# Optimization experiments

Measured on AMD Instinct MI355X. Metric: run time of the kernel, lower is better.

## Reference

```python
import jax, jax.numpy as jnp
import numpy as np

B, C, K, D = 16, 128, 128, 256
EPS = 1e-5  # torch BatchNorm1d default eps


def _bn(x, gamma, beta):
    # torch BatchNorm1d training-mode on (N, ch, L): normalize each channel over (N, L)
    mean = x.mean(axis=(0, 2), keepdims=True)
    var = x.var(axis=(0, 2), keepdims=True)  # biased, matches torch normalization
    return (x - mean) / jnp.sqrt(var + EPS) * gamma[None, :, None] + beta[None, :, None]


def setup_inputs() -> dict:
    key = jax.random.key(0)
    ks = jax.random.split(key, 6)
    q = jax.random.normal(ks[0], (B, C, D), jnp.float32)
    kc = jax.random.normal(ks[1], (B, K, D), jnp.float32)
    W0 = jax.random.normal(ks[2], (D, D), jnp.float32) / np.sqrt(D)
    W1 = jax.random.normal(ks[3], (D, D), jnp.float32) / np.sqrt(D)
    cmask = jax.random.randint(ks[4], (B, C), 0, 2, jnp.int32)
    kmask = jax.random.randint(ks[5], (B, K), 0, 2, jnp.int32)
    klen = jnp.maximum(kmask.sum(axis=1), 1).astype(jnp.int32)
    return {
        "query_candidates_repr": q,
        "key_candidates": kc,
        "W0": W0,
        "W1": W1,
        "bn0_gamma": jnp.ones((C,), jnp.float32),
        "bn0_beta": jnp.zeros((C,), jnp.float32),
        "bn1_gamma": jnp.ones((K,), jnp.float32),
        "bn1_beta": jnp.zeros((K,), jnp.float32),
        "query_candidate_mask": cmask,
        "key_candidate_mask": kmask,
        "key_candidate_len": klen,
    }


def reference(query_candidates_repr, key_candidates, W0, W1,
              bn0_gamma, bn0_beta, bn1_gamma, bn1_beta,
              query_candidate_mask, key_candidate_mask, key_candidate_len):
    # gated_attention branch (att_type != 'softmax'), activate = tanh
    g0 = _bn(query_candidates_repr @ W0.T, bn0_gamma, bn0_beta)  # (B,C,D)
    g1 = _bn(key_candidates @ W1.T, bn1_gamma, bn1_beta)          # (B,K,D)
    # (B,C,K,D) gate product
    attention_weight = jax.nn.sigmoid(g1)[:, None, :, :] * jax.nn.sigmoid(g0)[:, :, None, :]
    attention_res = key_candidates[:, None, :, :] * attention_weight  # (B,C,K,D)
    mask = (query_candidate_mask[:, :, None] * key_candidate_mask[:, None, :]).astype(jnp.float32)
    attention_res_masked = attention_res * mask[..., None]
    attention_vector = attention_res_masked.sum(axis=2) / key_candidate_len[:, None, None].astype(jnp.float32)
    output_res = jnp.tanh(attention_vector)  # (B,C,D)
    return output_res, attention_res_masked, attention_weight.mean(axis=-1)
```

## Files before the change

kernel.cpp:

```cpp
#include <hip/hip_runtime.h>


#define NB 16
#define NC 128
#define NK 128
#define ND 256

__global__ __launch_bounds__(256) void k_gemm(const float* __restrict__ q,
                                              const float* __restrict__ kc,
                                              const float* __restrict__ W0,
                                              const float* __restrict__ W1,
                                              float* __restrict__ Y) {
    __shared__ float As[16][64];
    __shared__ float Bs[16][64];
    const int m0 = blockIdx.x * 64;
    const int d0 = blockIdx.y * 64;
    const int t  = threadIdx.x;
    const float* A = (m0 < 2048) ? (q + (size_t)m0 * ND) : (kc + (size_t)(m0 - 2048) * ND);
    const float* W = (m0 < 2048) ? W0 : W1;
    const int ml = t >> 2;
    const int jl = (t & 3) * 4;
    const int ty = t >> 4;
    const int tx = t & 15;

    float acc[4][4] = {};
    for (int j0 = 0; j0 < 256; j0 += 16) {
        float4 a = *(const float4*)(A + ml * ND + j0 + jl);
        float4 b = *(const float4*)(W + (d0 + ml) * ND + j0 + jl);
        As[jl + 0][ml] = a.x; As[jl + 1][ml] = a.y; As[jl + 2][ml] = a.z; As[jl + 3][ml] = a.w;
        Bs[jl + 0][ml] = b.x; Bs[jl + 1][ml] = b.y; Bs[jl + 2][ml] = b.z; Bs[jl + 3][ml] = b.w;
        __syncthreads();
#pragma unroll
        for (int jj = 0; jj < 16; ++jj) {
            float4 av = *(const float4*)&As[jj][ty * 4];
            float4 bv = *(const float4*)&Bs[jj][tx * 4];
            acc[0][0] += av.x * bv.x; acc[0][1] += av.x * bv.y; acc[0][2] += av.x * bv.z; acc[0][3] += av.x * bv.w;
            acc[1][0] += av.y * bv.x; acc[1][1] += av.y * bv.y; acc[1][2] += av.y * bv.z; acc[1][3] += av.y * bv.w;
            acc[2][0] += av.z * bv.x; acc[2][1] += av.z * bv.y; acc[2][2] += av.z * bv.z; acc[2][3] += av.z * bv.w;
            acc[3][0] += av.w * bv.x; acc[3][1] += av.w * bv.y; acc[3][2] += av.w * bv.z; acc[3][3] += av.w * bv.w;
        }
        __syncthreads();
    }
#pragma unroll
    for (int i = 0; i < 4; ++i) {
        float4 o = make_float4(acc[i][0], acc[i][1], acc[i][2], acc[i][3]);
        *(float4*)(Y + (size_t)(m0 + ty * 4 + i) * ND + d0 + tx * 4) = o;
    }
}

__global__ __launch_bounds__(256) void k_stats(const float* __restrict__ Y,
                                               const float* __restrict__ g0, const float* __restrict__ b0,
                                               const float* __restrict__ g1, const float* __restrict__ b1,
                                               float* __restrict__ sc, float* __restrict__ sh) {
    const int ch = blockIdx.x;
    const int t  = threadIdx.x;
    const int rbase = (ch < 128) ? ch : (2048 + (ch - 128));
    float s = 0.f, s2 = 0.f;
#pragma unroll
    for (int b = 0; b < NB; ++b) {
        float v = Y[(size_t)(rbase + b * 128) * ND + t];
        s += v; s2 += v * v;
    }
#pragma unroll
    for (int off = 32; off > 0; off >>= 1) {
        s  += __shfl_down(s,  off, 64);
        s2 += __shfl_down(s2, off, 64);
    }
    __shared__ float r1[4], r2[4];
    const int w = t >> 6;
    if ((t & 63) == 0) { r1[w] = s; r2[w] = s2; }
    __syncthreads();
    if (t == 0) {
        s  = r1[0] + r1[1] + r1[2] + r1[3];
        s2 = r2[0] + r2[1] + r2[2] + r2[3];
        float mean = s * (1.f / 4096.f);
        float var  = s2 * (1.f / 4096.f) - mean * mean;
        float rstd = rsqrtf(var + 1e-5f);
        float g  = (ch < 128) ? g0[ch] : g1[ch - 128];
        float be = (ch < 128) ? b0[ch] : b1[ch - 128];
        sc[ch] = g * rstd;
        sh[ch] = be - mean * g * rstd;
    }
}

__global__ __launch_bounds__(256) void k_apply(float* __restrict__ Y,
                                               const float* __restrict__ sc, const float* __restrict__ sh) {
    const int m = blockIdx.x;
    const int t = threadIdx.x;
    const size_t idx = (size_t)m * ND + t;
    float x = Y[idx];
    const int ch = (m < 2048) ? (m & 127) : (128 + (m & 127));
    float g = x * sc[ch] + sh[ch];
    Y[idx] = 1.f / (1.f + __expf(-g));
}

__global__ __launch_bounds__(256) void k_big(const float* __restrict__ Y,
                                             const float* __restrict__ kc,
                                             const int* __restrict__ cmask,
                                             const int* __restrict__ kmask,
                                             const int* __restrict__ klen,
                                             float* __restrict__ out0,
                                             float* __restrict__ out1,
                                             float* __restrict__ out2) {
    const int bc = blockIdx.x;
    const int b  = bc >> 7;
    const int t  = threadIdx.x;
    const int f  = t & 63;
    const int g  = t >> 6;

    const float* s0row = Y + (size_t)bc * ND;
    const float* s1b   = Y + (size_t)(2048 + b * 128) * ND;
    const float* kcb   = kc + (size_t)b * 128 * ND;
    const int*   kmb   = kmask + b * 128;

    float4 s0v = *(const float4*)(s0row + f * 4);
    const bool cm = cmask[bc] != 0;
    float4 v0 = cm ? s0v : make_float4(0.f, 0.f, 0.f, 0.f);

    float tx_ = 0.f, ty_ = 0.f, tz_ = 0.f, tw_ = 0.f;
    const size_t o1base = (size_t)bc * 128 * ND;

    for (int k0 = 0; k0 < 32; ++k0) {
        const int k = k0 * 4 + g;
        float4 s1v = *(const float4*)(s1b + (size_t)k * ND + f * 4);
        float4 kcv = *(const float4*)(kcb + (size_t)k * ND + f * 4);
        const float km = (float)kmb[k];

        float4 uv = make_float4(km * kcv.x * s1v.x, km * kcv.y * s1v.y,
                                km * kcv.z * s1v.z, km * kcv.w * s1v.w);

        *(float4*)(out1 + o1base + (size_t)k * ND + f * 4) =
            make_float4(v0.x * uv.x, v0.y * uv.y, v0.z * uv.z, v0.w * uv.w);

        tx_ += uv.x; ty_ += uv.y; tz_ += uv.z; tw_ += uv.w;

        float dot = s0v.x * s1v.x + s0v.y * s1v.y + s0v.z * s1v.z + s0v.w * s1v.w;
#pragma unroll
        for (int off = 32; off > 0; off >>= 1) dot += __shfl_down(dot, off, 64);
        if (f == 0) out2[(size_t)bc * 128 + k] = dot * (1.f / 256.f);
    }

    __shared__ float tl[4][256];
    *(float4*)&tl[g][f * 4] = make_float4(tx_, ty_, tz_, tw_);
    __syncthreads();
    if (g == 0) {
        float4 t0 = *(const float4*)&tl[0][f * 4];
        float4 t1 = *(const float4*)&tl[1][f * 4];
        float4 t2 = *(const float4*)&tl[2][f * 4];
        float4 t3 = *(const float4*)&tl[3][f * 4];
        const float inv = 1.f / (float)klen[b];
        float ax = tanhf(v0.x * (t0.x + t1.x + t2.x + t3.x) * inv);
        float ay = tanhf(v0.y * (t0.y + t1.y + t2.y + t3.y) * inv);
        float az = tanhf(v0.z * (t0.z + t1.z + t2.z + t3.z) * inv);
        float aw = tanhf(v0.w * (t0.w + t1.w + t2.w + t3.w) * inv);
        *(float4*)(out0 + (size_t)bc * ND + f * 4) = make_float4(ax, ay, az, aw);
    }
}

extern "C" void kernel_launch(void* const* d_in, const int* in_sizes, int n_in,
                              void* d_out, int out_size, void* d_ws, size_t ws_size,
                              hipStream_t stream) {
    const float* q     = (const float*)d_in[0];
    const float* kc    = (const float*)d_in[1];
    const float* W0    = (const float*)d_in[2];
    const float* W1    = (const float*)d_in[3];
    const float* g0    = (const float*)d_in[4];
    const float* b0    = (const float*)d_in[5];
    const float* g1    = (const float*)d_in[6];
    const float* b1    = (const float*)d_in[7];
    const int*   cmask = (const int*)d_in[8];
    const int*   kmask = (const int*)d_in[9];
    const int*   klen  = (const int*)d_in[10];

    float* ws = (float*)d_ws;
    float* Y  = ws;
    float* sc = ws + 1048576;
    float* sh = ws + 1048832;

    float* o    = (float*)d_out;
    float* out0 = o;
    float* out1 = o + 524288;
    float* out2 = o + 67633152;

    k_gemm<<<dim3(64, 4), 256, 0, stream>>>(q, kc, W0, W1, Y);
    k_stats<<<256, 256, 0, stream>>>(Y, g0, b0, g1, b1, sc, sh);
    k_apply<<<4096, 256, 0, stream>>>(Y, sc, sh);
    k_big<<<2048, 256, 0, stream>>>(Y, kc, cmask, kmask, klen, out0, out1, out2);
}
```

Baseline: 321.6 us.

## Split big kernel: batched GEMM for gate mean, precompute masked key products

Moves the per-(c,k) gate-mean dot products out of the streaming kernel and computes them as a batched tiled GEMM. The masked key-candidate times sigmoid product and its per-batch sum over k are each precomputed once in their own small kernels instead of being recomputed per query row. The main kernel then only multiplies and streams the large attention_res output, using nontemporal stores. This removes the per-iteration shuffle reductions and redundant loads, at the cost of three extra launches.

```diff
diff --git a/kernel.cpp b/kernel.cpp
--- a/kernel.cpp
+++ b/kernel.cpp
@@ -5,6 +5,8 @@
 #define NC 128
 #define NK 128
 #define ND 256
+
+typedef float f4v __attribute__((ext_vector_type(4)));
 
 __global__ __launch_bounds__(256) void k_gemm(const float* __restrict__ q,
                                               const float* __restrict__ kc,
@@ -94,66 +96,107 @@
     Y[idx] = 1.f / (1.f + __expf(-g));
 }
 
-__global__ __launch_bounds__(256) void k_big(const float* __restrict__ Y,
-                                             const float* __restrict__ kc,
-                                             const int* __restrict__ cmask,
-                                             const int* __restrict__ kmask,
-                                             const int* __restrict__ klen,
-                                             float* __restrict__ out0,
-                                             float* __restrict__ out1,
-                                             float* __restrict__ out2) {
+__global__ __launch_bounds__(256) void k_out2(const float* __restrict__ Y,
+                                              float* __restrict__ out2) {
+    __shared__ float As[16][64];
+    __shared__ float Bs[16][64];
+    const int b  = blockIdx.z;
+    const int c0 = blockIdx.x * 64;
+    const int k0 = blockIdx.y * 64;
+    const int t  = threadIdx.x;
+    const float* A = Y + (size_t)(b * 128 + c0) * ND;
+    const float* W = Y + (size_t)(2048 + b * 128 + k0) * ND;
+    const int ml = t >> 2;
+    const int jl = (t & 3) * 4;
+    const int ty = t >> 4;
+    const int tx = t & 15;
+
+    float acc[4][4] = {};
+    for (int j0 = 0; j0 < 256; j0 += 16) {
+        float4 a = *(const float4*)(A + ml * ND + j0 + jl);
+        float4 bv_ = *(const float4*)(W + ml * ND + j0 + jl);
+        As[jl + 0][ml] = a.x; As[jl + 1][ml] = a.y; As[jl + 2][ml] = a.z; As[jl + 3][ml] = a.w;
+        Bs[jl + 0][ml] = bv_.x; Bs[jl + 1][ml] = bv_.y; Bs[jl + 2][ml] = bv_.z; Bs[jl + 3][ml] = bv_.w;
+        __syncthreads();
+#pragma unroll
+        for (int jj = 0; jj < 16; ++jj) {
+            float4 av = *(const float4*)&As[jj][ty * 4];
+            float4 bv = *(const float4*)&Bs[jj][tx * 4];
+            acc[0][0] += av.x * bv.x; acc[0][1] += av.x * bv.y; acc[0][2] += av.x * bv.z; acc[0][3] += av.x * bv.w;
+            acc[1][0] += av.y * bv.x; acc[1][1] += av.y * bv.y; acc[1][2] += av.y * bv.z; acc[1][3] += av.y * bv.w;
+            acc[2][0] += av.z * bv.x; acc[2][1] += av.z * bv.y; acc[2][2] += av.z * bv.z; acc[2][3] += av.z * bv.w;
+            acc[3][0] += av.w * bv.x; acc[3][1] += av.w * bv.y; acc[3][2] += av.w * bv.z; acc[3][3] += av.w * bv.w;
+        }
+        __syncthreads();
+    }
+    const float scale = 1.f / 256.f;
+#pragma unroll
+    for (int i = 0; i < 4; ++i) {
+        float4 o = make_float4(acc[i][0] * scale, acc[i][1] * scale, acc[i][2] * scale, acc[i][3] * scale);
+        *(float4*)(out2 + ((size_t)(b * 128 + c0 + ty * 4 + i)) * 128 + k0 + tx * 4) = o;
+    }
+}
+
+__global__ __launch_bounds__(256) void k_u(float* __restrict__ Y,
+                                           const float* __restrict__ kc,
+                                           const int* __restrict__ kmask) {
+    const int r = blockIdx.x;
+    const int t = threadIdx.x;
+    const size_t idx = (size_t)(2048 + r) * ND + t;
+    const float km = (float)kmask[r];
+    Y[idx] = km * kc[(size_t)r * ND + t] * Y[idx];
+}
+
+__global__ __launch_bounds__(256) void k_t(const float* __restrict__ Y,
+                                           float* __restrict__ tvec) {
+    const int b = blockIdx.x;
+    const int t = threadIdx.x;
+    const float* u = Y + (size_t)(2048 + b * 128) * ND;
+    float s0 = 0.f, s1 = 0.f, s2 = 0.f, s3 = 0.f;
+#pragma unroll 8
+    for (int k = 0; k < 128; k += 4) {
+        s0 += u[(size_t)(k + 0) * ND + t];
+        s1 += u[(size_t)(k + 1) * ND + t];
+        s2 += u[(size_t)(k + 2) * ND + t];
+        s3 += u[(size_t)(k + 3) * ND + t];
+    }
+    tvec[b * ND + t] = (s0 + s1) + (s2 + s3);
+}
+
+__global__ __launch_bounds__(256) void k_big2(const float* __restrict__ Y,
+                                              const float* __restrict__ tvec,
+                                              const int* __restrict__ cmask,
+                                              const int* __restrict__ klen,
+                                              float* __restrict__ out0,
+                                              float* __restrict__ out1) {
     const int bc = blockIdx.x;
     const int b  = bc >> 7;
     const int t  = threadIdx.x;
     const int f  = t & 63;
     const int g  = t >> 6;
 
-    const float* s0row = Y + (size_t)bc * ND;
-    const float* s1b   = Y + (size_t)(2048 + b * 128) * ND;
-    const float* kcb   = kc + (size_t)b * 128 * ND;
-    const int*   kmb   = kmask + b * 128;
-
-    float4 s0v = *(const float4*)(s0row + f * 4);
+    float4 s0v = *(const float4*)(Y + (size_t)bc * ND + f * 4);
     const bool cm = cmask[bc] != 0;
     float4 v0 = cm ? s0v : make_float4(0.f, 0.f, 0.f, 0.f);
 
-    float tx_ = 0.f, ty_ = 0.f, tz_ = 0.f, tw_ = 0.f;
-    const size_t o1base = (size_t)bc * 128 * ND;
-
+    const float* up = Y + (size_t)(2048 + b * 128 + g) * ND + f * 4;
+    float*       op = out1 + (size_t)bc * 128 * ND + (size_t)g * ND + f * 4;
+
+#pragma unroll 4
     for (int k0 = 0; k0 < 32; ++k0) {
-        const int k = k0 * 4 + g;
-        float4 s1v = *(const float4*)(s1b + (size_t)k * ND + f * 4);
-        float4 kcv = *(const float4*)(kcb + (size_t)k * ND + f * 4);
-        const float km = (float)kmb[k];
-
-        float4 uv = make_float4(km * kcv.x * s1v.x, km * kcv.y * s1v.y,
-                                km * kcv.z * s1v.z, km * kcv.w * s1v.w);
-
-        *(float4*)(out1 + o1base + (size_t)k * ND + f * 4) =
-            make_float4(v0.x * uv.x, v0.y * uv.y, v0.z * uv.z, v0.w * uv.w);
-
-        tx_ += uv.x; ty_ += uv.y; tz_ += uv.z; tw_ += uv.w;
-
-        float dot = s0v.x * s1v.x + s0v.y * s1v.y + s0v.z * s1v.z + s0v.w * s1v.w;
-#pragma unroll
-        for (int off = 32; off > 0; off >>= 1) dot += __shfl_down(dot, off, 64);
-        if (f == 0) out2[(size_t)bc * 128 + k] = dot * (1.f / 256.f);
-    }
-
-    __shared__ float tl[4][256];
-    *(float4*)&tl[g][f * 4] = make_float4(tx_, ty_, tz_, tw_);
-    __syncthreads();
+        float4 uv = *(const float4*)up;
+        float4 o = make_float4(v0.x * uv.x, v0.y * uv.y, v0.z * uv.z, v0.w * uv.w);
+        __builtin_nontemporal_store(*(const f4v*)&o, (f4v*)op);
+        up += 4 * ND;
+        op += 4 * ND;
+    }
+
     if (g == 0) {
-        float4 t0 = *(const float4*)&tl[0][f * 4];
-        float4 t1 = *(const float4*)&tl[1][f * 4];
-        float4 t2 = *(const float4*)&tl[2][f * 4];
-        float4 t3 = *(const float4*)&tl[3][f * 4];
+        float4 tv = *(const float4*)(tvec + b * ND + f * 4);
         const float inv = 1.f / (float)klen[b];
-        float ax = tanhf(v0.x * (t0.x + t1.x + t2.x + t3.x) * inv);
-        float ay = tanhf(v0.y * (t0.y + t1.y + t2.y + t3.y) * inv);
-        float az = tanhf(v0.z * (t0.z + t1.z + t2.z + t3.z) * inv);
-        float aw = tanhf(v0.w * (t0.w + t1.w + t2.w + t3.w) * inv);
-        *(float4*)(out0 + (size_t)bc * ND + f * 4) = make_float4(ax, ay, az, aw);
+        float4 o0 = make_float4(tanhf(v0.x * tv.x * inv), tanhf(v0.y * tv.y * inv),
+                                tanhf(v0.z * tv.z * inv), tanhf(v0.w * tv.w * inv));
+        *(float4*)(out0 + (size_t)bc * ND + f * 4) = o0;
     }
 }
 
@@ -176,14 +219,18 @@
     float* Y  = ws;
     float* sc = ws + 1048576;
     float* sh = ws + 1048832;
+    float* tv = ws + 1049088;
 
     float* o    = (float*)d_out;
     float* out0 = o;
     float* out1 = o + 524288;
     float* out2 = o + 67633152;
 
-    k_gemm<<<dim3(64, 4), 256, 0, stream>>>(q, kc, W0, W1, Y);
-    k_stats<<<256, 256, 0, stream>>>(Y, g0, b0, g1, b1, sc, sh);
-    k_apply<<<4096, 256, 0, stream>>>(Y, sc, sh);
-    k_big<<<2048, 256, 0, stream>>>(Y, kc, cmask, kmask, klen, out0, out1, out2);
-}
+    k_gemm <<<dim3(64, 4),    256, 0, stream>>>(q, kc, W0, W1, Y);
+    k_stats<<<256,            256, 0, stream>>>(Y, g0, b0, g1, b1, sc, sh);
+    k_apply<<<4096,           256, 0, stream>>>(Y, sc, sh);
+    k_out2 <<<dim3(2, 2, 16), 256, 0, stream>>>(Y, out2);
+    k_u    <<<2048,           256, 0, stream>>>(Y, kc, kmask);
+    k_t    <<<16,             256, 0, stream>>>(Y, tv);
+    k_big2 <<<2048,           256, 0, stream>>>(Y, tv, cmask, klen, out0, out1);
+}
```

Result: slower. 335.4 us (+4.3%).
